# Performance work log

Measured on AMD Instinct MI355X. Metric: run time of the kernel, lower is better.

## Reference

```python
import jax, jax.numpy as jnp
import numpy as np

B, S, H = 2, 2048, 2048
INTER = 1024
N_ROUTED = 8
ZERO = 4
TOTAL = N_ROUTED + ZERO
TOP_K = 2
SCALE = 1.5


def setup_inputs() -> dict:
    key = jax.random.key(0)
    k0, k1, k2, k3, k4, k5 = jax.random.split(key, 6)
    w = 0.02  # weight init scale
    return {
        "hidden_states": jax.random.normal(k0, (B, S, H), jnp.float32),
        "classifier_w": jax.random.normal(k1, (TOTAL, H), jnp.float32) * w,
        "e_score_correction_bias": jax.random.normal(k2, (TOTAL,), jnp.float32) * w,
        "gate_w": jax.random.normal(k3, (N_ROUTED, INTER, H), jnp.float32) * w,
        "up_w": jax.random.normal(k4, (N_ROUTED, INTER, H), jnp.float32) * w,
        "down_w": jax.random.normal(k5, (N_ROUTED, H, INTER), jnp.float32) * w,
    }


def reference(hidden_states, classifier_w, e_score_correction_bias, gate_w, up_w, down_w):
    x = hidden_states  # [B,S,H]
    total = classifier_w.shape[0]
    n_routed = gate_w.shape[0]

    # --- Router: softmax over all experts, bias only for selection ---
    logits = jnp.einsum('bsh,eh->bse', x, classifier_w)          # [B,S,total]
    probs = jax.nn.softmax(logits, axis=-1)
    biased = probs + e_score_correction_bias
    _, idx = jax.lax.top_k(biased, TOP_K)                         # [B,S,K] int
    rw = jnp.take_along_axis(probs, idx, axis=-1) * SCALE         # unbiased probs as weights

    # Dense per-expert weight via one-hot combine (Equal+Mul+ReduceSum in original)
    w_full = jnp.sum(jax.nn.one_hot(idx, total, dtype=x.dtype) * rw[..., None], axis=-2)  # [B,S,total]

    # --- Compute ALL routed experts densely (matches original op graph) ---
    g = jnp.einsum('bsh,eih->bsei', x, gate_w)                    # [B,S,E,INTER]
    u = jnp.einsum('bsh,eih->bsei', x, up_w)
    act = jax.nn.silu(g) * u
    expert_out = jnp.einsum('bsei,ehi->bseh', act, down_w)        # [B,S,E,H]

    out = jnp.einsum('bse,bseh->bsh', w_full[..., :n_routed], expert_out)
    # Zero (identity) experts pass hidden_states through
    out = out + x * jnp.sum(w_full[..., n_routed:], axis=-1, keepdims=True)
    return out
```

## Files before the change

### kernel.cpp

```cpp
#include <hip/hip_runtime.h>
#include <cstdint>

#define T_TOKENS 4096
#define HDIM 2048
#define IDIM 1024
#define NEXP 8
#define NTOT 12
#define MAX_SLOTS 8320

typedef __bf16 bf16x8_t __attribute__((ext_vector_type(8)));
typedef float f32x4_t __attribute__((ext_vector_type(4)));
typedef unsigned short u16x8_t __attribute__((ext_vector_type(8)));
typedef unsigned short u16x4_t __attribute__((ext_vector_type(4)));

__device__ __forceinline__ unsigned short f2bf(float f) {
    unsigned int u = __builtin_bit_cast(unsigned int, f);
    u += 0x7fffu + ((u >> 16) & 1u);
    return (unsigned short)(u >> 16);
}
__device__ __forceinline__ float bfu2f(unsigned short u) {
    unsigned int v = ((unsigned int)u) << 16;
    return __builtin_bit_cast(float, v);
}
__device__ __forceinline__ void async16(const unsigned short* g, unsigned short* l) {
    __builtin_amdgcn_global_load_lds(
        (const unsigned int __attribute__((address_space(1)))*)g,
        (unsigned int __attribute__((address_space(3)))*)l,
        16, 0, 0);
}
__device__ __forceinline__ void cvt16(const float* src, unsigned short* dst) {
    f32x4_t f0 = ((const f32x4_t*)src)[0];
    f32x4_t f1 = ((const f32x4_t*)src)[1];
    f32x4_t f2 = ((const f32x4_t*)src)[2];
    f32x4_t f3 = ((const f32x4_t*)src)[3];
    u16x8_t a, b;
#pragma unroll
    for (int j = 0; j < 4; ++j) { a[j] = f2bf(f0[j]); a[4 + j] = f2bf(f1[j]); }
#pragma unroll
    for (int j = 0; j < 4; ++j) { b[j] = f2bf(f2[j]); b[4 + j] = f2bf(f3[j]); }
    ((u16x8_t*)dst)[0] = a;
    ((u16x8_t*)dst)[1] = b;
}

__global__ void init_kernel(int* __restrict__ meta) {
    int i = threadIdx.x;
    if (i < 32) meta[i] = 0;
}

__global__ void noop_kernel() {}

__global__ void pack_w_kernel(const float* __restrict__ gw, const float* __restrict__ uw,
                              const float* __restrict__ dw,
                              unsigned short* __restrict__ guwb,
                              unsigned short* __restrict__ dwb) {
    const int n8_gu = NEXP * 2 * IDIM * HDIM / 8;
    const int n8_d = NEXP * HDIM * IDIM / 8;
    int stride = gridDim.x * blockDim.x;
    for (int i = blockIdx.x * blockDim.x + threadIdx.x; i < n8_gu + n8_d; i += stride) {
        if (i < n8_gu) {
            size_t f = (size_t)i * 8;
            int h = (int)(f & (HDIM - 1));
            int p = (int)((f >> 11) & 2047);
            int e = (int)(f >> 22);
            int j = p >> 5, r = p & 31;
            const float* base = (r < 16) ? gw : uw;
            const float* src = base + ((size_t)e * IDIM + 16 * j + (r & 15)) * HDIM + h;
            f32x4_t a = ((const f32x4_t*)src)[0];
            f32x4_t b = ((const f32x4_t*)src)[1];
            u16x8_t o;
#pragma unroll
            for (int q = 0; q < 4; ++q) { o[q] = f2bf(a[q]); o[4 + q] = f2bf(b[q]); }
            ((u16x8_t*)guwb)[i] = o;
        } else {
            int k = i - n8_gu;
            const f32x4_t* p4 = (const f32x4_t*)(dw + (size_t)k * 8);
            f32x4_t a = p4[0], b = p4[1];
            u16x8_t o;
#pragma unroll
            for (int q = 0; q < 4; ++q) { o[q] = f2bf(a[q]); o[4 + q] = f2bf(b[q]); }
            ((u16x8_t*)dwb)[k] = o;
        }
    }
}

__global__ void router_kernel(const float* __restrict__ x,
                              const float* __restrict__ cw,
                              const float* __restrict__ bias,
                              int* __restrict__ counts,
                              int* __restrict__ tok_e,
                              float* __restrict__ tok_w,
                              float* __restrict__ zero_w,
                              unsigned short* __restrict__ xb) {
    const int token = blockIdx.x;
    const int ln = threadIdx.x;
    const float* xr = x + (size_t)token * HDIM;
    float acc[NTOT];
#pragma unroll
    for (int e = 0; e < NTOT; ++e) acc[e] = 0.f;
    for (int h0 = ln * 4; h0 < HDIM; h0 += 256) {
        f32x4_t xv = *(const f32x4_t*)(xr + h0);
        if (xb) {
            u16x4_t o;
#pragma unroll
            for (int j = 0; j < 4; ++j) o[j] = f2bf(xv[j]);
            *(u16x4_t*)(xb + (size_t)token * HDIM + h0) = o;
        }
#pragma unroll
        for (int e = 0; e < NTOT; ++e) {
            f32x4_t wv = *(const f32x4_t*)(cw + e * HDIM + h0);
            acc[e] += xv[0] * wv[0] + xv[1] * wv[1] + xv[2] * wv[2] + xv[3] * wv[3];
        }
    }
#pragma unroll
    for (int e = 0; e < NTOT; ++e) {
        float v = acc[e];
#pragma unroll
        for (int s = 32; s > 0; s >>= 1) v += __shfl_xor(v, s, 64);
        acc[e] = v;
    }
    if (ln == 0) {
        float mx = acc[0];
#pragma unroll
        for (int e = 1; e < NTOT; ++e) mx = fmaxf(mx, acc[e]);
        float p[NTOT];
        float sum = 0.f;
#pragma unroll
        for (int e = 0; e < NTOT; ++e) { p[e] = __expf(acc[e] - mx); sum += p[e]; }
        float inv = 1.f / sum;
#pragma unroll
        for (int e = 0; e < NTOT; ++e) p[e] *= inv;
        float b[NTOT];
#pragma unroll
        for (int e = 0; e < NTOT; ++e) b[e] = p[e] + bias[e];
        int i0 = 0; float v0 = b[0];
#pragma unroll
        for (int e = 1; e < NTOT; ++e) if (b[e] > v0) { v0 = b[e]; i0 = e; }
        int i1 = -1; float v1 = -3.0e38f;
#pragma unroll
        for (int e = 0; e < NTOT; ++e) if (e != i0 && b[e] > v1) { v1 = b[e]; i1 = e; }
        if (i1 < 0) i1 = (i0 == 0) ? 1 : 0;
        float w0 = p[i0] * 1.5f, w1 = p[i1] * 1.5f;
        tok_e[2 * token] = i0; tok_e[2 * token + 1] = i1;
        tok_w[2 * token] = w0; tok_w[2 * token + 1] = w1;
        float zw = 0.f;
        if (i0 >= NEXP) zw += w0; else atomicAdd(&counts[i0], 1);
        if (i1 >= NEXP) zw += w1; else atomicAdd(&counts[i1], 1);
        zero_w[token] = zw;
    }
}

__global__ void scan_kernel(const int* __restrict__ counts, int* __restrict__ offs) {
    if (threadIdx.x == 0 && blockIdx.x == 0) {
        int a = 0;
        for (int e = 0; e < NEXP; ++e) {
            offs[e] = a;
            int c = counts[e];
            if (c < 0) c = 0;
            if (c > T_TOKENS) c = T_TOKENS;
            a += c;
        }
        if (a > 2 * T_TOKENS) a = 2 * T_TOKENS;
        offs[NEXP] = a;
    }
}

__global__ void place_kernel(const int* __restrict__ tok_e, const float* __restrict__ tok_w,
                             const int* __restrict__ offs, int* __restrict__ fill,
                             int* __restrict__ token_list, float* __restrict__ slot_w,
                             int* __restrict__ map) {
    int token = blockIdx.x * blockDim.x + threadIdx.x;
    if (token >= T_TOKENS) return;
#pragma unroll
    for (int j = 0; j < 2; ++j) {
        int e = tok_e[2 * token + j];
        int m = -1;
        if (e >= 0 && e < NEXP) {
            int pos = atomicAdd(&fill[e], 1);
            int slot = offs[e] + pos;
            if (slot >= 0 && slot < 2 * T_TOKENS) {
                token_list[slot] = token;
                slot_w[slot] = tok_w[2 * token + j];
                m = slot;
            }
        }
        map[2 * token + j] = m;
    }
}

__launch_bounds__(256, 3)
__global__ void gemm1_kernel(const unsigned short* __restrict__ xb,
                             const unsigned short* __restrict__ guwb,
                             const int* __restrict__ offs,
                             const int* __restrict__ token_list,
                             const float* __restrict__ slot_w,
                             unsigned short* __restrict__ act) {
    const int e = blockIdx.z;
    const int off = offs[e];
    int Me = offs[e + 1] - off;
    if (Me < 0) Me = 0;
    if (Me > T_TOKENS) Me = T_TOKENS;
    const int m0 = blockIdx.y * 128;
    if (m0 >= Me) return;
    const int n0 = blockIdx.x * 128;

    __shared__ __align__(16) unsigned short As[128][32];
    __shared__ __align__(16) unsigned short Bs[128][32];

    const int tid = threadIdx.x;
    const int wv = tid >> 6, ln = tid & 63;
    const int sc = (ln & 3) * 8;

    int tr0 = m0 + wv * 16 + (ln >> 2);      if (tr0 >= Me) tr0 = Me - 1;
    int tr1 = m0 + 64 + wv * 16 + (ln >> 2); if (tr1 >= Me) tr1 = Me - 1;
    int tok0 = token_list[off + tr0]; if (tok0 < 0 || tok0 >= T_TOKENS) tok0 = 0;
    int tok1 = token_list[off + tr1]; if (tok1 < 0 || tok1 >= T_TOKENS) tok1 = 0;
    const unsigned short* aA0 = xb + (size_t)tok0 * HDIM + sc;
    const unsigned short* aA1 = xb + (size_t)tok1 * HDIM + sc;
    unsigned short* lA0 = &As[wv * 16][0];
    unsigned short* lA1 = &As[64 + wv * 16][0];

    const unsigned short* aB0 = guwb + (size_t)e * 2 * IDIM * HDIM +
                                (size_t)(n0 + wv * 16 + (ln >> 2)) * HDIM + sc;
    const unsigned short* aB1 = aB0 + (size_t)64 * HDIM;
    unsigned short* lB0 = &Bs[wv * 16][0];
    unsigned short* lB1 = &Bs[64 + wv * 16][0];

    const int wm = wv & 1, wn = wv >> 1;
    const int fr = ln & 15;
    const int fk = (ln >> 4) * 8;

    f32x4_t acc[4][4] = {};

    for (int k0 = 0; k0 < HDIM; k0 += 32) {
        async16(aA0 + k0, lA0);
        async16(aA1 + k0, lA1);
        async16(aB0 + k0, lB0);
        async16(aB1 + k0, lB1);
        __syncthreads();
        bf16x8_t af[4], bfr[4];
#pragma unroll
        for (int t = 0; t < 4; ++t) {
            af[t] = *(const bf16x8_t*)&As[wm * 64 + t * 16 + fr][fk];
            bfr[t] = *(const bf16x8_t*)&Bs[wn * 64 + t * 16 + fr][fk];
        }
#pragma unroll
        for (int mt = 0; mt < 4; ++mt)
#pragma unroll
            for (int nt = 0; nt < 4; ++nt)
                acc[mt][nt] = __builtin_amdgcn_mfma_f32_16x16x32_bf16(af[mt], bfr[nt], acc[mt][nt], 0, 0, 0);
        __syncthreads();
    }

    const int ibase = (n0 >> 1) + wn * 32;
#pragma unroll
    for (int mt = 0; mt < 4; ++mt) {
#pragma unroll
        for (int r = 0; r < 4; ++r) {
            int rloc = wm * 64 + mt * 16 + (ln >> 4) * 4 + r;
            int grow = m0 + rloc;
            if (grow < Me) {
                float w = slot_w[off + grow];
                size_t rb = (size_t)(off + grow) * IDIM + ibase;
#pragma unroll
                for (int t = 0; t < 2; ++t) {
                    float g = acc[mt][2 * t][r];
                    float u = acc[mt][2 * t + 1][r];
                    float s = g / (1.f + __expf(-g));
                    act[rb + t * 16 + fr] = f2bf(s * u * w);
                }
            }
        }
    }
}

__launch_bounds__(256, 3)
__global__ void gemm2_kernel(const unsigned short* __restrict__ act,
                             const unsigned short* __restrict__ dwb,
                             const int* __restrict__ offs,
                             unsigned short* __restrict__ dout) {
    const int e = blockIdx.z;
    const int off = offs[e];
    int Me = offs[e + 1] - off;
    if (Me < 0) Me = 0;
    if (Me > T_TOKENS) Me = T_TOKENS;
    const int m0 = blockIdx.y * 128;
    if (m0 >= Me) return;
    const int n0 = blockIdx.x * 128;

    __shared__ __align__(16) unsigned short As[128][32];
    __shared__ __align__(16) unsigned short Bs[128][32];

    const int tid = threadIdx.x;
    const int wv = tid >> 6, ln = tid & 63;
    const int sc = (ln & 3) * 8;

    const int sr = wv * 16 + (ln >> 2);
    int ar0 = off + m0 + sr;      if (ar0 >= MAX_SLOTS) ar0 = MAX_SLOTS - 1;
    int ar1 = off + m0 + 64 + sr; if (ar1 >= MAX_SLOTS) ar1 = MAX_SLOTS - 1;
    const unsigned short* aA0 = act + (size_t)ar0 * IDIM + sc;
    const unsigned short* aA1 = act + (size_t)ar1 * IDIM + sc;
    unsigned short* lA0 = &As[wv * 16][0];
    unsigned short* lA1 = &As[64 + wv * 16][0];

    const unsigned short* aB0 = dwb + (size_t)e * HDIM * IDIM +
                                (size_t)(n0 + wv * 16 + (ln >> 2)) * IDIM + sc;
    const unsigned short* aB1 = aB0 + (size_t)64 * IDIM;
    unsigned short* lB0 = &Bs[wv * 16][0];
    unsigned short* lB1 = &Bs[64 + wv * 16][0];

    const int wm = wv & 1, wn = wv >> 1;
    const int fr = ln & 15;
    const int fk = (ln >> 4) * 8;

    f32x4_t acc[4][4] = {};

    for (int k0 = 0; k0 < IDIM; k0 += 32) {
        async16(aA0 + k0, lA0);
        async16(aA1 + k0, lA1);
        async16(aB0 + k0, lB0);
        async16(aB1 + k0, lB1);
        __syncthreads();
        bf16x8_t af[4], bfr[4];
#pragma unroll
        for (int t = 0; t < 4; ++t) {
            af[t] = *(const bf16x8_t*)&As[wm * 64 + t * 16 + fr][fk];
            bfr[t] = *(const bf16x8_t*)&Bs[wn * 64 + t * 16 + fr][fk];
        }
#pragma unroll
        for (int mt = 0; mt < 4; ++mt)
#pragma unroll
            for (int nt = 0; nt < 4; ++nt)
                acc[mt][nt] = __builtin_amdgcn_mfma_f32_16x16x32_bf16(af[mt], bfr[nt], acc[mt][nt], 0, 0, 0);
        __syncthreads();
    }

#pragma unroll
    for (int mt = 0; mt < 4; ++mt) {
#pragma unroll
        for (int r = 0; r < 4; ++r) {
            int rloc = wm * 64 + mt * 16 + (ln >> 4) * 4 + r;
            int grow = m0 + rloc;
            if (grow < Me) {
                size_t rb = (size_t)(off + grow) * HDIM + n0;
#pragma unroll
                for (int nt = 0; nt < 4; ++nt)
                    dout[rb + wn * 64 + nt * 16 + fr] = f2bf(acc[mt][nt][r]);
            }
        }
    }
}

__launch_bounds__(256, 2)
__global__ void gemm1_fb(const float* __restrict__ x,
                         const float* __restrict__ gate_w,
                         const float* __restrict__ up_w,
                         const int* __restrict__ offs,
                         const int* __restrict__ token_list,
                         const float* __restrict__ slot_w,
                         unsigned short* __restrict__ act) {
    const int e = blockIdx.z;
    const int off = offs[e];
    int Me = offs[e + 1] - off;
    if (Me < 0) Me = 0;
    if (Me > T_TOKENS) Me = T_TOKENS;
    const int m0 = blockIdx.y * 128;
    if (m0 >= Me) return;
    const int n0 = blockIdx.x * 128;

    __shared__ __align__(16) unsigned short As[128][32];
    __shared__ __align__(16) unsigned short Gs[128][32];
    __shared__ __align__(16) unsigned short Us[128][32];

    const int tid = threadIdx.x;
    const int srow = tid >> 1;
    const int shalf = (tid & 1) * 16;

    int tr = m0 + srow; if (tr >= Me) tr = Me - 1;
    int tok = token_list[off + tr];
    if (tok < 0 || tok >= T_TOKENS) tok = 0;
    const float* aA = x + (size_t)tok * HDIM + shalf;
    const float* aG = gate_w + (size_t)e * IDIM * HDIM + (size_t)(n0 + srow) * HDIM + shalf;
    const float* aU = up_w + (size_t)e * IDIM * HDIM + (size_t)(n0 + srow) * HDIM + shalf;
    unsigned short* lA = &As[srow][shalf];
    unsigned short* lG = &Gs[srow][shalf];
    unsigned short* lU = &Us[srow][shalf];

    const int wv = tid >> 6, ln = tid & 63;
    const int wm = wv & 1, wn = wv >> 1;
    const int fr = ln & 15;
    const int fk = (ln >> 4) * 8;

    f32x4_t accg[4][4] = {};
    f32x4_t accu[4][4] = {};

    for (int k0 = 0; k0 < HDIM; k0 += 32) {
        cvt16(aA + k0, lA);
        cvt16(aG + k0, lG);
        cvt16(aU + k0, lU);
        __syncthreads();
        bf16x8_t af[4], gf[4], uf[4];
#pragma unroll
        for (int t = 0; t < 4; ++t) {
            af[t] = *(const bf16x8_t*)&As[wm * 64 + t * 16 + fr][fk];
            gf[t] = *(const bf16x8_t*)&Gs[wn * 64 + t * 16 + fr][fk];
            uf[t] = *(const bf16x8_t*)&Us[wn * 64 + t * 16 + fr][fk];
        }
#pragma unroll
        for (int mt = 0; mt < 4; ++mt)
#pragma unroll
            for (int nt = 0; nt < 4; ++nt) {
                accg[mt][nt] = __builtin_amdgcn_mfma_f32_16x16x32_bf16(af[mt], gf[nt], accg[mt][nt], 0, 0, 0);
                accu[mt][nt] = __builtin_amdgcn_mfma_f32_16x16x32_bf16(af[mt], uf[nt], accu[mt][nt], 0, 0, 0);
            }
        __syncthreads();
    }

#pragma unroll
    for (int mt = 0; mt < 4; ++mt) {
#pragma unroll
        for (int r = 0; r < 4; ++r) {
            int rloc = wm * 64 + mt * 16 + (ln >> 4) * 4 + r;
            int grow = m0 + rloc;
            if (grow < Me) {
                float w = slot_w[off + grow];
                size_t rb = (size_t)(off + grow) * IDIM + n0;
#pragma unroll
                for (int nt = 0; nt < 4; ++nt) {
                    float g = accg[mt][nt][r];
                    float u = accu[mt][nt][r];
                    float s = g / (1.f + __expf(-g));
                    act[rb + wn * 64 + nt * 16 + fr] = f2bf(s * u * w);
                }
            }
        }
    }
}

__launch_bounds__(256, 2)
__global__ void gemm2_fb(const unsigned short* __restrict__ act,
                         const float* __restrict__ dwn,
                         const int* __restrict__ offs,
                         unsigned short* __restrict__ dout) {
    const int e = blockIdx.z;
    const int off = offs[e];
    int Me = offs[e + 1] - off;
    if (Me < 0) Me = 0;
    if (Me > T_TOKENS) Me = T_TOKENS;
    const int m0 = blockIdx.y * 128;
    if (m0 >= Me) return;
    const int n0 = blockIdx.x * 128;

    __shared__ __align__(16) unsigned short As[128][32];
    __shared__ __align__(16) unsigned short Bs[128][32];

    const int tid = threadIdx.x;
    const int wv = tid >> 6, ln = tid & 63;

    const int sr0 = wv * 16 + (ln >> 2);
    const int sc = (ln & 3) * 8;
    int ar0 = off + m0 + sr0;      if (ar0 >= MAX_SLOTS) ar0 = MAX_SLOTS - 1;
    int ar1 = off + m0 + 64 + sr0; if (ar1 >= MAX_SLOTS) ar1 = MAX_SLOTS - 1;
    const unsigned short* aA0 = act + (size_t)ar0 * IDIM + sc;
    const unsigned short* aA1 = act + (size_t)ar1 * IDIM + sc;
    unsigned short* lA0 = &As[wv * 16][0];
    unsigned short* lA1 = &As[64 + wv * 16][0];

    const int srow = tid >> 1;
    const int shalf = (tid & 1) * 16;
    const float* aB = dwn + (size_t)e * HDIM * IDIM + (size_t)(n0 + srow) * IDIM + shalf;
    unsigned short* lB = &Bs[srow][shalf];

    const int wm = wv & 1, wn = wv >> 1;
    const int fr = ln & 15;
    const int fk = (ln >> 4) * 8;

    f32x4_t acc[4][4] = {};

    for (int k0 = 0; k0 < IDIM; k0 += 32) {
        async16(aA0 + k0, lA0);
        async16(aA1 + k0, lA1);
        cvt16(aB + k0, lB);
        __syncthreads();
        bf16x8_t af[4], bfr[4];
#pragma unroll
        for (int t = 0; t < 4; ++t) {
            af[t] = *(const bf16x8_t*)&As[wm * 64 + t * 16 + fr][fk];
            bfr[t] = *(const bf16x8_t*)&Bs[wn * 64 + t * 16 + fr][fk];
        }
#pragma unroll
        for (int mt = 0; mt < 4; ++mt)
#pragma unroll
            for (int nt = 0; nt < 4; ++nt)
                acc[mt][nt] = __builtin_amdgcn_mfma_f32_16x16x32_bf16(af[mt], bfr[nt], acc[mt][nt], 0, 0, 0);
        __syncthreads();
    }

#pragma unroll
    for (int mt = 0; mt < 4; ++mt) {
#pragma unroll
        for (int r = 0; r < 4; ++r) {
            int rloc = wm * 64 + mt * 16 + (ln >> 4) * 4 + r;
            int grow = m0 + rloc;
            if (grow < Me) {
                size_t rb = (size_t)(off + grow) * HDIM + n0;
#pragma unroll
                for (int nt = 0; nt < 4; ++nt)
                    dout[rb + wn * 64 + nt * 16 + fr] = f2bf(acc[mt][nt][r]);
            }
        }
    }
}

__global__ void finalize_kernel(const float* __restrict__ x,
                                const unsigned short* __restrict__ dout,
                                const int* __restrict__ map,
                                const float* __restrict__ zero_w,
                                float* __restrict__ out) {
    int gid = blockIdx.x * blockDim.x + threadIdx.x;
    int token = gid >> 8;
    int hg = (gid & 255) * 8;
    int s0 = map[2 * token], s1 = map[2 * token + 1];
    float zw = zero_w[token];
    size_t base = (size_t)token * HDIM + hg;
    f32x4_t x0 = *(const f32x4_t*)(x + base);
    f32x4_t x1 = *(const f32x4_t*)(x + base + 4);
    float o[8];
#pragma unroll
    for (int j = 0; j < 4; ++j) { o[j] = zw * x0[j]; o[4 + j] = zw * x1[j]; }
    if (s0 >= 0 && s0 < 2 * T_TOKENS) {
        u16x8_t d = *(const u16x8_t*)(dout + (size_t)s0 * HDIM + hg);
#pragma unroll
        for (int j = 0; j < 8; ++j) o[j] += bfu2f(d[j]);
    }
    if (s1 >= 0 && s1 < 2 * T_TOKENS) {
        u16x8_t d = *(const u16x8_t*)(dout + (size_t)s1 * HDIM + hg);
#pragma unroll
        for (int j = 0; j < 8; ++j) o[j] += bfu2f(d[j]);
    }
    f32x4_t o0, o1;
#pragma unroll
    for (int j = 0; j < 4; ++j) { o0[j] = o[j]; o1[j] = o[4 + j]; }
    *(f32x4_t*)(out + base) = o0;
    *(f32x4_t*)(out + base + 4) = o1;
}

extern "C" void kernel_launch(void* const* d_in, const int* in_sizes, int n_in,
                              void* d_out, int out_size, void* d_ws, size_t ws_size,
                              hipStream_t stream) {
    const float* x = (const float*)d_in[0];
    const float* cw = (const float*)d_in[1];
    const float* bias = (const float*)d_in[2];
    const float* gw = (const float*)d_in[3];
    const float* uw = (const float*)d_in[4];
    const float* dw = (const float*)d_in[5];
    float* out = (float*)d_out;

    char* ws = (char*)d_ws;
    int* counts = (int*)(ws + 0);
    int* fill = (int*)(ws + 32);
    int* offs = (int*)(ws + 64);
    int* tok_e = (int*)(ws + 128);
    float* tok_w = (float*)(ws + 32896);
    float* zero_w = (float*)(ws + 65664);
    int* map = (int*)(ws + 82048);
    int* token_list = (int*)(ws + 114816);
    float* slot_w = (float*)(ws + 148096);
    unsigned short* act = (unsigned short*)(ws + 181504);
    unsigned short* dout = (unsigned short*)(ws + 17220864);
    const size_t needed_small = 51299584ull;
    unsigned short* xb   = (unsigned short*)(ws + 51299584ull);
    unsigned short* guwb = (unsigned short*)(ws + 68076800ull);
    unsigned short* dwb  = (unsigned short*)(ws + 135185664ull);
    const size_t needed_big = 168740096ull;

    if (ws_size < needed_small) {
        noop_kernel<<<1, 64, 0, stream>>>();
        return;
    }

    init_kernel<<<1, 64, 0, stream>>>((int*)ws);

    if (ws_size >= needed_big) {
        router_kernel<<<T_TOKENS, 64, 0, stream>>>(x, cw, bias, counts, tok_e, tok_w, zero_w, xb);
        scan_kernel<<<1, 64, 0, stream>>>(counts, offs);
        place_kernel<<<(T_TOKENS + 255) / 256, 256, 0, stream>>>(tok_e, tok_w, offs, fill,
                                                                 token_list, slot_w, map);
        pack_w_kernel<<<4096, 256, 0, stream>>>(gw, uw, dw, guwb, dwb);
        gemm1_kernel<<<dim3(2 * IDIM / 128, 32, NEXP), 256, 0, stream>>>(xb, guwb, offs,
                                                                         token_list, slot_w, act);
        gemm2_kernel<<<dim3(HDIM / 128, 32, NEXP), 256, 0, stream>>>(act, dwb, offs, dout);
    } else {
        router_kernel<<<T_TOKENS, 64, 0, stream>>>(x, cw, bias, counts, tok_e, tok_w, zero_w,
                                                   (unsigned short*)nullptr);
        scan_kernel<<<1, 64, 0, stream>>>(counts, offs);
        place_kernel<<<(T_TOKENS + 255) / 256, 256, 0, stream>>>(tok_e, tok_w, offs, fill,
                                                                 token_list, slot_w, map);
        gemm1_fb<<<dim3(IDIM / 128, 32, NEXP), 256, 0, stream>>>(x, gw, uw, offs,
                                                                 token_list, slot_w, act);
        gemm2_fb<<<dim3(HDIM / 128, 32, NEXP), 256, 0, stream>>>(act, dw, offs, dout);
    }

    finalize_kernel<<<(T_TOKENS * HDIM / 8 + 255) / 256, 256, 0, stream>>>(x, dout, map,
                                                                           zero_w, out);
}
```

Baseline: 500.4 us.

## Fuse fp32-to-bf16 weight conversion into GEMM tile loads, drop pack kernel

```diff
diff --git a/kernel.cpp b/kernel.cpp
--- a/kernel.cpp
+++ b/kernel.cpp
@@ -28,6 +28,12 @@
         (unsigned int __attribute__((address_space(3)))*)l,
         16, 0, 0);
 }
+__device__ __forceinline__ void async16f(const float* g, float* l) {
+    __builtin_amdgcn_global_load_lds(
+        (const unsigned int __attribute__((address_space(1)))*)g,
+        (unsigned int __attribute__((address_space(3)))*)l,
+        16, 0, 0);
+}
 __device__ __forceinline__ void cvt16(const float* src, unsigned short* dst) {
     f32x4_t f0 = ((const f32x4_t*)src)[0];
     f32x4_t f1 = ((const f32x4_t*)src)[1];
@@ -48,40 +54,6 @@
 }
 
 __global__ void noop_kernel() {}
-
-__global__ void pack_w_kernel(const float* __restrict__ gw, const float* __restrict__ uw,
-                              const float* __restrict__ dw,
-                              unsigned short* __restrict__ guwb,
-                              unsigned short* __restrict__ dwb) {
-    const int n8_gu = NEXP * 2 * IDIM * HDIM / 8;
-    const int n8_d = NEXP * HDIM * IDIM / 8;
-    int stride = gridDim.x * blockDim.x;
-    for (int i = blockIdx.x * blockDim.x + threadIdx.x; i < n8_gu + n8_d; i += stride) {
-        if (i < n8_gu) {
-            size_t f = (size_t)i * 8;
-            int h = (int)(f & (HDIM - 1));
-            int p = (int)((f >> 11) & 2047);
-            int e = (int)(f >> 22);
-            int j = p >> 5, r = p & 31;
-            const float* base = (r < 16) ? gw : uw;
-            const float* src = base + ((size_t)e * IDIM + 16 * j + (r & 15)) * HDIM + h;
-            f32x4_t a = ((const f32x4_t*)src)[0];
-            f32x4_t b = ((const f32x4_t*)src)[1];
-            u16x8_t o;
-#pragma unroll
-            for (int q = 0; q < 4; ++q) { o[q] = f2bf(a[q]); o[4 + q] = f2bf(b[q]); }
-            ((u16x8_t*)guwb)[i] = o;
-        } else {
-            int k = i - n8_gu;
-            const f32x4_t* p4 = (const f32x4_t*)(dw + (size_t)k * 8);
-            f32x4_t a = p4[0], b = p4[1];
-            u16x8_t o;
-#pragma unroll
-            for (int q = 0; q < 4; ++q) { o[q] = f2bf(a[q]); o[4 + q] = f2bf(b[q]); }
-            ((u16x8_t*)dwb)[k] = o;
-        }
-    }
-}
 
 __global__ void router_kernel(const float* __restrict__ x,
                               const float* __restrict__ cw,
@@ -189,7 +161,8 @@
 
 __launch_bounds__(256, 3)
 __global__ void gemm1_kernel(const unsigned short* __restrict__ xb,
-                             const unsigned short* __restrict__ guwb,
+                             const float* __restrict__ gate_w,
+                             const float* __restrict__ up_w,
                              const int* __restrict__ offs,
                              const int* __restrict__ token_list,
                              const float* __restrict__ slot_w,
@@ -204,14 +177,15 @@
     const int n0 = blockIdx.x * 128;
 
     __shared__ __align__(16) unsigned short As[128][32];
-    __shared__ __align__(16) unsigned short Bs[128][32];
+    __shared__ __align__(16) float Bsf[128][32];
 
     const int tid = threadIdx.x;
     const int wv = tid >> 6, ln = tid & 63;
     const int sc = (ln & 3) * 8;
-
-    int tr0 = m0 + wv * 16 + (ln >> 2);      if (tr0 >= Me) tr0 = Me - 1;
-    int tr1 = m0 + 64 + wv * 16 + (ln >> 2); if (tr1 >= Me) tr1 = Me - 1;
+    const int R = ln >> 2;
+
+    int tr0 = m0 + wv * 16 + R;      if (tr0 >= Me) tr0 = Me - 1;
+    int tr1 = m0 + 64 + wv * 16 + R; if (tr1 >= Me) tr1 = Me - 1;
     int tok0 = token_list[off + tr0]; if (tok0 < 0 || tok0 >= T_TOKENS) tok0 = 0;
     int tok1 = token_list[off + tr1]; if (tok1 < 0 || tok1 >= T_TOKENS) tok1 = 0;
     const unsigned short* aA0 = xb + (size_t)tok0 * HDIM + sc;
@@ -219,29 +193,42 @@
     unsigned short* lA0 = &As[wv * 16][0];
     unsigned short* lA1 = &As[64 + wv * 16][0];
 
-    const unsigned short* aB0 = guwb + (size_t)e * 2 * IDIM * HDIM +
-                                (size_t)(n0 + wv * 16 + (ln >> 2)) * HDIM + sc;
-    const unsigned short* aB1 = aB0 + (size_t)64 * HDIM;
-    unsigned short* lB0 = &Bs[wv * 16][0];
-    unsigned short* lB1 = &Bs[64 + wv * 16][0];
+    const float* wsel = (wv < 2) ? gate_w : up_w;
+    const float* aB = wsel + ((size_t)e * IDIM + (n0 >> 1) + (wv & 1) * 8 + (ln >> 3)) * HDIM
+                      + (((ln & 7) ^ (ln >> 3)) * 4);
+    float* lB0 = &Bsf[wv * 8][0];
+    float* lB1 = &Bsf[32 + wv * 8][0];
+    float* lB2 = &Bsf[64 + wv * 8][0];
+    float* lB3 = &Bsf[96 + wv * 8][0];
 
     const int wm = wv & 1, wn = wv >> 1;
     const int fr = ln & 15;
     const int fk = (ln >> 4) * 8;
+    const int cb0 = fk >> 2;
 
     f32x4_t acc[4][4] = {};
 
     for (int k0 = 0; k0 < HDIM; k0 += 32) {
         async16(aA0 + k0, lA0);
         async16(aA1 + k0, lA1);
-        async16(aB0 + k0, lB0);
-        async16(aB1 + k0, lB1);
+        async16f(aB + k0, lB0);
+        async16f(aB + (size_t)16 * HDIM + k0, lB1);
+        async16f(aB + (size_t)32 * HDIM + k0, lB2);
+        async16f(aB + (size_t)48 * HDIM + k0, lB3);
         __syncthreads();
         bf16x8_t af[4], bfr[4];
 #pragma unroll
         for (int t = 0; t < 4; ++t) {
             af[t] = *(const bf16x8_t*)&As[wm * 64 + t * 16 + fr][fk];
-            bfr[t] = *(const bf16x8_t*)&Bs[wn * 64 + t * 16 + fr][fk];
+            const int row = wn * 64 + t * 16 + fr;
+            const int rx = row & 7;
+            f32x4_t lo = *(const f32x4_t*)&Bsf[row][(cb0 ^ rx) * 4];
+            f32x4_t hi = *(const f32x4_t*)&Bsf[row][((cb0 + 1) ^ rx) * 4];
+#pragma unroll
+            for (int j = 0; j < 4; ++j) {
+                bfr[t][j] = (__bf16)lo[j];
+                bfr[t][4 + j] = (__bf16)hi[j];
+            }
         }
 #pragma unroll
         for (int mt = 0; mt < 4; ++mt)
@@ -275,7 +262,7 @@
 
 __launch_bounds__(256, 3)
 __global__ void gemm2_kernel(const unsigned short* __restrict__ act,
-                             const unsigned short* __restrict__ dwb,
+                             const float* __restrict__ dwn,
                              const int* __restrict__ offs,
                              unsigned short* __restrict__ dout) {
     const int e = blockIdx.z;
@@ -288,43 +275,55 @@
     const int n0 = blockIdx.x * 128;
 
     __shared__ __align__(16) unsigned short As[128][32];
-    __shared__ __align__(16) unsigned short Bs[128][32];
+    __shared__ __align__(16) float Bsf[128][32];
 
     const int tid = threadIdx.x;
     const int wv = tid >> 6, ln = tid & 63;
     const int sc = (ln & 3) * 8;
-
-    const int sr = wv * 16 + (ln >> 2);
-    int ar0 = off + m0 + sr;      if (ar0 >= MAX_SLOTS) ar0 = MAX_SLOTS - 1;
-    int ar1 = off + m0 + 64 + sr; if (ar1 >= MAX_SLOTS) ar1 = MAX_SLOTS - 1;
+    const int R = ln >> 2;
+
+    int ar0 = off + m0 + wv * 16 + R;      if (ar0 >= MAX_SLOTS) ar0 = MAX_SLOTS - 1;
+    int ar1 = off + m0 + 64 + wv * 16 + R; if (ar1 >= MAX_SLOTS) ar1 = MAX_SLOTS - 1;
     const unsigned short* aA0 = act + (size_t)ar0 * IDIM + sc;
     const unsigned short* aA1 = act + (size_t)ar1 * IDIM + sc;
     unsigned short* lA0 = &As[wv * 16][0];
     unsigned short* lA1 = &As[64 + wv * 16][0];
 
-    const unsigned short* aB0 = dwb + (size_t)e * HDIM * IDIM +
-                                (size_t)(n0 + wv * 16 + (ln >> 2)) * IDIM + sc;
-    const unsigned short* aB1 = aB0 + (size_t)64 * IDIM;
-    unsigned short* lB0 = &Bs[wv * 16][0];
-    unsigned short* lB1 = &Bs[64 + wv * 16][0];
+    const float* aB = dwn + (size_t)e * HDIM * IDIM +
+                      (size_t)(n0 + wv * 8 + (ln >> 3)) * IDIM + (((ln & 7) ^ (ln >> 3)) * 4);
+    float* lB0 = &Bsf[wv * 8][0];
+    float* lB1 = &Bsf[32 + wv * 8][0];
+    float* lB2 = &Bsf[64 + wv * 8][0];
+    float* lB3 = &Bsf[96 + wv * 8][0];
 
     const int wm = wv & 1, wn = wv >> 1;
     const int fr = ln & 15;
     const int fk = (ln >> 4) * 8;
+    const int cb0 = fk >> 2;
 
     f32x4_t acc[4][4] = {};
 
     for (int k0 = 0; k0 < IDIM; k0 += 32) {
         async16(aA0 + k0, lA0);
         async16(aA1 + k0, lA1);
-        async16(aB0 + k0, lB0);
-        async16(aB1 + k0, lB1);
+        async16f(aB + k0, lB0);
+        async16f(aB + (size_t)32 * IDIM + k0, lB1);
+        async16f(aB + (size_t)64 * IDIM + k0, lB2);
+        async16f(aB + (size_t)96 * IDIM + k0, lB3);
         __syncthreads();
         bf16x8_t af[4], bfr[4];
 #pragma unroll
         for (int t = 0; t < 4; ++t) {
             af[t] = *(const bf16x8_t*)&As[wm * 64 + t * 16 + fr][fk];
-            bfr[t] = *(const bf16x8_t*)&Bs[wn * 64 + t * 16 + fr][fk];
+            const int row = wn * 64 + t * 16 + fr;
+            const int rx = row & 7;
+            f32x4_t lo = *(const f32x4_t*)&Bsf[row][(cb0 ^ rx) * 4];
+            f32x4_t hi = *(const f32x4_t*)&Bsf[row][((cb0 + 1) ^ rx) * 4];
+#pragma unroll
+            for (int j = 0; j < 4; ++j) {
+                bfr[t][j] = (__bf16)lo[j];
+                bfr[t][4 + j] = (__bf16)hi[j];
+            }
         }
 #pragma unroll
         for (int mt = 0; mt < 4; ++mt)
@@ -568,10 +567,8 @@
     unsigned short* act = (unsigned short*)(ws + 181504);
     unsigned short* dout = (unsigned short*)(ws + 17220864);
     const size_t needed_small = 51299584ull;
-    unsigned short* xb   = (unsigned short*)(ws + 51299584ull);
-    unsigned short* guwb = (unsigned short*)(ws + 68076800ull);
-    unsigned short* dwb  = (unsigned short*)(ws + 135185664ull);
-    const size_t needed_big = 168740096ull;
+    unsigned short* xb = (unsigned short*)(ws + 51299584ull);
+    const size_t needed_big = 68076800ull;
 
     if (ws_size < needed_small) {
         noop_kernel<<<1, 64, 0, stream>>>();
@@ -585,10 +582,9 @@
         scan_kernel<<<1, 64, 0, stream>>>(counts, offs);
         place_kernel<<<(T_TOKENS + 255) / 256, 256, 0, stream>>>(tok_e, tok_w, offs, fill,
                                                                  token_list, slot_w, map);
-        pack_w_kernel<<<4096, 256, 0, stream>>>(gw, uw, dw, guwb, dwb);
-        gemm1_kernel<<<dim3(2 * IDIM / 128, 32, NEXP), 256, 0, stream>>>(xb, guwb, offs,
+        gemm1_kernel<<<dim3(2 * IDIM / 128, 32, NEXP), 256, 0, stream>>>(xb, gw, uw, offs,
                                                                          token_list, slot_w, act);
-        gemm2_kernel<<<dim3(HDIM / 128, 32, NEXP), 256, 0, stream>>>(act, dwb, offs, dout);
+        gemm2_kernel<<<dim3(HDIM / 128, 32, NEXP), 256, 0, stream>>>(act, dw, offs, dout);
     } else {
         router_kernel<<<T_TOKENS, 64, 0, stream>>>(x, cw, bias, counts, tok_e, tok_w, zero_w,
                                                    (unsigned short*)nullptr);
```

New measurement: 491.7 us. About the same (-1.7%).
